# Kernel optimization log

Hardware: AMD Instinct MI355X
Metric: run time of the kernel (lower is better)

## Reference

```python
import jax, jax.numpy as jnp
import numpy as np

T, H, E = 1024, 2048, 32
I = 1024            # moe_intermediate_size
K = 8               # num_experts_per_token
G = 4               # num_expert_group
TOPK_GROUP = 2
N_SHARED = 2
IS = I * N_SHARED   # shared-expert intermediate
RSF = 2.5           # routed_scaling_factor


def setup_inputs() -> dict:
    key = jax.random.key(0)
    ks = jax.random.split(key, 9)
    s = 0.02
    return {
        "hidden_states": jax.random.normal(ks[0], (T, H), jnp.float32),
        "gate_w": jax.random.normal(ks[1], (H, E), jnp.float32) * s,
        "corr_bias": jax.random.normal(ks[2], (E,), jnp.float32) * s,
        "w_gate": jax.random.normal(ks[3], (E, H, I), jnp.float32) * s,
        "w_up": jax.random.normal(ks[4], (E, H, I), jnp.float32) * s,
        "w_down": jax.random.normal(ks[5], (E, I, H), jnp.float32) * s,
        "sw_gate": jax.random.normal(ks[6], (H, IS), jnp.float32) * s,
        "sw_up": jax.random.normal(ks[7], (H, IS), jnp.float32) * s,
        "sw_down": jax.random.normal(ks[8], (IS, H), jnp.float32) * s,
    }


def _route(x, gate_w, corr_bias):
    # biased grouped top-k (DeepSeek-V3 style sigmoid routing)
    logits = x @ gate_w                      # [T,E]
    scores = jax.nn.sigmoid(logits)
    sfc = scores + corr_bias[None, :]        # scores for choice
    grp = sfc.reshape(-1, G, E // G)
    # group score = sum of top-2 biased scores within the group
    grp_score = jax.lax.top_k(grp, 2)[0].sum(-1)          # [T,G]
    _, gidx = jax.lax.top_k(grp_score, TOPK_GROUP)        # [T,topk_group]
    rows = jnp.arange(sfc.shape[0])[:, None]
    gmask = jnp.zeros((sfc.shape[0], G), sfc.dtype).at[rows, gidx].set(1.0)
    emask = jnp.repeat(gmask, E // G, axis=1)             # [T,E]
    masked = jnp.where(emask > 0, sfc, -jnp.inf)
    _, idx = jax.lax.top_k(masked, K)                     # [T,K]
    w = jnp.take_along_axis(scores, idx, axis=1)          # unbiased scores
    w = w / w.sum(-1, keepdims=True)                      # renormalize
    w = w * RSF                                           # routed scaling
    combine = jnp.zeros((sfc.shape[0], E), x.dtype).at[rows, idx].add(w)
    return combine                                        # dense [T,E] combine weights


def reference(hidden_states, gate_w, corr_bias, w_gate, w_up, w_down,
              sw_gate, sw_up, sw_down):
    x = hidden_states
    # shared experts (SiLU-gated MLP)
    shared = (jax.nn.silu(x @ sw_gate) * (x @ sw_up)) @ sw_down   # [T,H]
    # routing
    combine = _route(x, gate_w, corr_bias)                        # [T,E]
    # routed experts (dense grouped-GEMM reference)
    g = jnp.einsum('th,ehi->tei', x, w_gate)
    u = jnp.einsum('th,ehi->tei', x, w_up)
    a = jax.nn.silu(g) * u                                        # [T,E,I]
    y = jnp.einsum('tei,eih->teh', a, w_down)                     # [T,E,H]
    routed = jnp.einsum('teh,te->th', y, combine)
    return routed + shared
```

## Files before the change

### kernel.cpp

```cpp
#include <hip/hip_runtime.h>

#define T_TOK 1024
#define H_DIM 2048
#define E_NUM 32
#define I_DIM 1024
#define IS_DIM 2048

typedef float  f32x4 __attribute__((ext_vector_type(4)));
typedef short  s16x8 __attribute__((ext_vector_type(8)));
typedef unsigned short u16x4 __attribute__((ext_vector_type(4)));
typedef unsigned short u16x8 __attribute__((ext_vector_type(8)));

__device__ __forceinline__ unsigned short f2bf(float f) {
    unsigned u = __builtin_bit_cast(unsigned, f);
    u = (u + 0x7fffu + ((u >> 16) & 1u)) >> 16;
    return (unsigned short)u;
}

__device__ __forceinline__ int swz(int r, int c) {
    return (r << 5) + (c ^ (((r >> 2) & 3) << 3));
}

__global__ __launch_bounds__(256) void cvt_k(
    const float* __restrict__ x, unsigned short* __restrict__ xb)
{
    const int i = (blockIdx.x * 256 + threadIdx.x) * 8;
    f32x4 a = *(const f32x4*)(x + i);
    f32x4 b = *(const f32x4*)(x + i + 4);
    u16x8 h = { f2bf(a[0]), f2bf(a[1]), f2bf(a[2]), f2bf(a[3]),
                f2bf(b[0]), f2bf(b[1]), f2bf(b[2]), f2bf(b[3]) };
    *(u16x8*)(xb + i) = h;
}

__global__ __launch_bounds__(256) void route_k(
    const float* __restrict__ x, const float* __restrict__ gw,
    const float* __restrict__ bias, int* __restrict__ tidx,
    float* __restrict__ tw)
{
    const int w = threadIdx.x >> 6;
    const int lane = threadIdx.x & 63;
    const int t = blockIdx.x * 4 + w;
    __shared__ float xs[4][H_DIM];
    __shared__ float sfc[4][E_NUM];
    __shared__ float sc[4][E_NUM];

    for (int i = threadIdx.x; i < 4 * (H_DIM / 4); i += 256) {
        int tt = i >> 9;
        int c = i & 511;
        *(f32x4*)&xs[tt][c * 4] =
            *(const f32x4*)(x + (size_t)(blockIdx.x * 4 + tt) * H_DIM + c * 4);
    }
    __syncthreads();

    const int eq = (lane & 7) * 4;
    const int hs = lane >> 3;
    f32x4 acc = {0.f, 0.f, 0.f, 0.f};
    #pragma unroll 4
    for (int h = hs; h < H_DIM; h += 8) {
        float xv = xs[w][h];
        f32x4 gv = *(const f32x4*)(gw + (size_t)h * E_NUM + eq);
        acc += gv * xv;
    }
    #pragma unroll
    for (int m = 8; m < 64; m <<= 1) {
        acc[0] += __shfl_xor(acc[0], m);
        acc[1] += __shfl_xor(acc[1], m);
        acc[2] += __shfl_xor(acc[2], m);
        acc[3] += __shfl_xor(acc[3], m);
    }
    if (lane < 8) {
        #pragma unroll
        for (int j = 0; j < 4; ++j) {
            float s = 1.f / (1.f + expf(-acc[j]));
            sc[w][eq + j] = s;
            sfc[w][eq + j] = s + bias[eq + j];
        }
    }
    __syncthreads();

    if (lane == 0) {
        float gs[4];
        for (int gg = 0; gg < 4; ++gg) {
            float m1 = -1e30f, m2 = -1e30f;
            for (int j = 0; j < 8; ++j) {
                float v = sfc[w][gg * 8 + j];
                if (v > m1) { m2 = m1; m1 = v; }
                else if (v > m2) { m2 = v; }
            }
            gs[gg] = m1 + m2;
        }
        int g1 = 0;
        for (int gg = 1; gg < 4; ++gg) if (gs[gg] > gs[g1]) g1 = gg;
        int g2 = (g1 == 0) ? 1 : 0;
        for (int gg = 0; gg < 4; ++gg)
            if (gg != g1 && gs[gg] > gs[g2]) g2 = gg;

        unsigned allow = (0xFFu << (g1 * 8)) | (0xFFu << (g2 * 8));
        unsigned taken = 0u;
        int   isel[8];
        float wsel[8];
        float wsum = 0.f;
        for (int k = 0; k < 8; ++k) {
            int best = 0; float bv = -1e30f;
            for (int e2 = 0; e2 < 32; ++e2) {
                if (((allow >> e2) & 1u) && !((taken >> e2) & 1u)) {
                    float v = sfc[w][e2];
                    if (v > bv) { bv = v; best = e2; }
                }
            }
            taken |= 1u << best;
            isel[k] = best;
            wsel[k] = sc[w][best];
            wsum += sc[w][best];
        }
        const float f = 2.5f / wsum;
        for (int k = 0; k < 8; ++k) {
            tidx[t * 8 + k] = isel[k];
            tw[t * 8 + k] = wsel[k] * f;
        }
    }
}

__global__ __launch_bounds__(64) void build_k(
    const int* __restrict__ tidx, const float* __restrict__ tw,
    int* __restrict__ ltok, float* __restrict__ lw, int* __restrict__ counts)
{
    const int e = blockIdx.x;
    const int lane = threadIdx.x;
    int cnt = 0;
    for (int t0 = 0; t0 < T_TOK; t0 += 64) {
        const int t = t0 + lane;
        int sel = 0; float w = 0.f;
        #pragma unroll
        for (int k = 0; k < 8; ++k) {
            if (tidx[t * 8 + k] == e) { sel = 1; w = tw[t * 8 + k]; }
        }
        unsigned long long m = __ballot(sel);
        int pos = __popcll(m & ((1ull << lane) - 1ull));
        if (sel) {
            ltok[e * T_TOK + cnt + pos] = t;
            lw[e * T_TOK + cnt + pos] = w;
        }
        cnt += __popcll(m);
    }
    if (lane == 0) counts[e] = cnt;
}

__global__ void prefix_k(const int* __restrict__ counts, int* __restrict__ offsets)
{
    if (threadIdx.x == 0) {
        int off = 0;
        for (int e = 0; e < E_NUM; ++e) { offsets[e] = off; off += counts[e]; }
    }
}

template<int DUAL, int EXPERT, int GATHER, int ATOMIC, int BM>
__global__ __launch_bounds__(256, 4) void gemm_k(
    const unsigned short* __restrict__ A, const float* __restrict__ B1g,
    const float* __restrict__ B2g, void* __restrict__ outv,
    const int* __restrict__ counts, const int* __restrict__ offsets,
    const int* __restrict__ ltok, const float* __restrict__ lw,
    int M, int N, int K)
{
    constexpr int WR  = BM / 2;
    constexpr int FM  = WR / 16;
    constexpr int TPR = 256 / BM;
    constexpr int KSP = 32 / TPR;
    constexpr int NB  = KSP / 8;

    const int e = blockIdx.z;
    const int Mloc = EXPERT ? counts[e] : M;
    const int col0 = blockIdx.y * 64;
    const int rb = EXPERT ? offsets[e] : 0;

    const float* B1 = B1g;
    const float* B2 = B2g;
    if (EXPERT) {
        size_t eo = (size_t)e * K * N;
        B1 += eo;
        if (DUAL) B2 += eo;
    }

    __shared__ unsigned short lA[2][BM * 32];
    __shared__ unsigned short lB[2][DUAL + 1][64 * 32];

    const int tid = threadIdx.x;
    const int lane = tid & 63;
    const int wv = tid >> 6;
    const int wm = wv >> 1;
    const int wn = wv & 1;

    const int arow = tid / TPR;
    const int akb  = (tid % TPR) * KSP;

    const bool doB = tid < (DUAL ? 256 : 128);
    const int bmat = DUAL ? (tid >> 7) : 0;
    const int t7 = tid & 127;
    const int nq = t7 & 15;
    const int kq = t7 >> 4;
    const float* bp = (bmat ? B2 : B1) + (size_t)(4 * kq) * N + col0 + nq * 4;

    f32x4 acc1[FM][2], acc2[FM][2];
    u16x8 pbaX[NB], pbaY[NB];
    f32x4 pbX[4], pbY[4];
    const unsigned short* apb = nullptr;

    auto loadT = [&](int k0, u16x8 (&pba)[NB], f32x4 (&pb)[4]) {
        #pragma unroll
        for (int i = 0; i < NB; ++i)
            pba[i] = *(const u16x8*)(apb + k0 + i * 8);
        if (doB) {
            #pragma unroll
            for (int j = 0; j < 4; ++j)
                pb[j] = *(const f32x4*)(bp + (size_t)(k0 + j) * N);
        }
    };

    auto storeT = [&](int p, u16x8 (&pba)[NB], f32x4 (&pb)[4]) {
        #pragma unroll
        for (int i = 0; i < NB; ++i)
            *(u16x8*)&lA[p][swz(arow, akb + i * 8)] = pba[i];
        if (doB) {
            #pragma unroll
            for (int j2 = 0; j2 < 4; ++j2) {
                u16x4 h = { f2bf(pb[0][j2]), f2bf(pb[1][j2]),
                            f2bf(pb[2][j2]), f2bf(pb[3][j2]) };
                *(u16x4*)&lB[p][bmat][swz(nq * 4 + j2, kq * 4)] = h;
            }
        }
    };

    auto compute = [&](int p) {
        const int koff = (lane >> 4) * 8;
        s16x8 af[FM], b1f[2], b2f[2];
        #pragma unroll
        for (int fm = 0; fm < FM; ++fm)
            af[fm] = *(const s16x8*)&lA[p][swz(wm * WR + fm * 16 + (lane & 15), koff)];
        #pragma unroll
        for (int fn = 0; fn < 2; ++fn) {
            b1f[fn] = *(const s16x8*)&lB[p][0][swz(wn * 32 + fn * 16 + (lane & 15), koff)];
            if (DUAL)
                b2f[fn] = *(const s16x8*)&lB[p][1][swz(wn * 32 + fn * 16 + (lane & 15), koff)];
        }
        #pragma unroll
        for (int fm = 0; fm < FM; ++fm)
            #pragma unroll
            for (int fn = 0; fn < 2; ++fn) {
                acc1[fm][fn] = __builtin_amdgcn_mfma_f32_16x16x32_bf16(
                    af[fm], b1f[fn], acc1[fm][fn], 0, 0, 0);
                if (DUAL)
                    acc2[fm][fn] = __builtin_amdgcn_mfma_f32_16x16x32_bf16(
                        af[fm], b2f[fn], acc2[fm][fn], 0, 0, 0);
            }
    };

    const int nk = K >> 5;

    for (int row0 = blockIdx.x * BM; row0 < Mloc; row0 += gridDim.x * BM) {
        {
            int rr = row0 + arow;
            if (rr >= Mloc) rr = Mloc - 1;
            int grow = GATHER ? ltok[e * T_TOK + rr] : (rb + rr);
            apb = A + (size_t)grow * K + akb;
        }
        #pragma unroll
        for (int a = 0; a < FM; ++a)
            #pragma unroll
            for (int b = 0; b < 2; ++b) {
                acc1[a][b] = f32x4{0.f, 0.f, 0.f, 0.f};
                acc2[a][b] = f32x4{0.f, 0.f, 0.f, 0.f};
            }

        loadT(0, pbaX, pbX);
        loadT(32, pbaY, pbY);
        __syncthreads();
        storeT(0, pbaX, pbX);
        __syncthreads();

        for (int kt = 0; kt < nk; kt += 2) {
            if (kt + 2 < nk) loadT((kt + 2) << 5, pbaX, pbX);
            compute(0);
            storeT(1, pbaY, pbY);
            __syncthreads();
            if (kt + 3 < nk) loadT((kt + 3) << 5, pbaY, pbY);
            compute(1);
            if (kt + 2 < nk) {
                storeT(0, pbaX, pbX);
                __syncthreads();
            }
        }

        const int fr = (lane >> 4) << 2;
        const int fc = lane & 15;
        if (DUAL) {
            unsigned short* outp = (unsigned short*)outv;
            #pragma unroll
            for (int fm = 0; fm < FM; ++fm)
                #pragma unroll
                for (int fn = 0; fn < 2; ++fn)
                    #pragma unroll
                    for (int j = 0; j < 4; ++j) {
                        int r = wm * WR + fm * 16 + fr + j;
                        if (row0 + r < Mloc) {
                            int cc = col0 + wn * 32 + fn * 16 + fc;
                            float gv = acc1[fm][fn][j];
                            float uv = acc2[fm][fn][j];
                            float a = gv / (1.f + expf(-gv)) * uv;
                            outp[(size_t)(rb + row0 + r) * N + cc] = f2bf(a);
                        }
                    }
        } else if (ATOMIC) {
            float* outp = (float*)outv;
            #pragma unroll
            for (int fm = 0; fm < FM; ++fm)
                #pragma unroll
                for (int fn = 0; fn < 2; ++fn)
                    #pragma unroll
                    for (int j = 0; j < 4; ++j) {
                        int r = wm * WR + fm * 16 + fr + j;
                        if (row0 + r < Mloc) {
                            int tok = ltok[e * T_TOK + row0 + r];
                            float wr = lw[e * T_TOK + row0 + r];
                            int cc = col0 + wn * 32 + fn * 16 + fc;
                            atomicAdd(outp + (size_t)tok * N + cc, acc1[fm][fn][j] * wr);
                        }
                    }
        } else {
            float* outp = (float*)outv;
            #pragma unroll
            for (int fm = 0; fm < FM; ++fm)
                #pragma unroll
                for (int fn = 0; fn < 2; ++fn)
                    #pragma unroll
                    for (int j = 0; j < 4; ++j) {
                        int r = wm * WR + fm * 16 + fr + j;
                        if (row0 + r < Mloc) {
                            int cc = col0 + wn * 32 + fn * 16 + fc;
                            outp[(size_t)(row0 + r) * N + cc] = acc1[fm][fn][j];
                        }
                    }
        }
    }
}

extern "C" void kernel_launch(void* const* d_in, const int* in_sizes, int n_in,
                              void* d_out, int out_size, void* d_ws, size_t ws_size,
                              hipStream_t stream) {
    const float* x       = (const float*)d_in[0];
    const float* gate_w  = (const float*)d_in[1];
    const float* bias    = (const float*)d_in[2];
    const float* w_gate  = (const float*)d_in[3];
    const float* w_up    = (const float*)d_in[4];
    const float* w_down  = (const float*)d_in[5];
    const float* sw_gate = (const float*)d_in[6];
    const float* sw_up   = (const float*)d_in[7];
    const float* sw_down = (const float*)d_in[8];
    float* out = (float*)d_out;

    char* ws = (char*)d_ws;
    int*   topk_idx = (int*)ws;
    float* topk_w   = (float*)(ws + 32768);
    int*   counts   = (int*)(ws + 65536);
    int*   offsets  = (int*)(ws + 65536 + 128);
    int*   ltok     = (int*)(ws + 65536 + 256);
    float* lw       = (float*)(ws + 65536 + 256 + 131072);
    unsigned short* act_s = (unsigned short*)(ws + 65536 + 256 + 262144);
    unsigned short* act_r = act_s + (size_t)T_TOK * IS_DIM;
    unsigned short* xbf   = act_r + (size_t)T_TOK * 8 * I_DIM;

    cvt_k<<<T_TOK * H_DIM / 2048, 256, 0, stream>>>(x, xbf);
    route_k<<<T_TOK / 4, 256, 0, stream>>>(x, gate_w, bias, topk_idx, topk_w);
    build_k<<<E_NUM, 64, 0, stream>>>(topk_idx, topk_w, ltok, lw, counts);
    prefix_k<<<1, 64, 0, stream>>>(counts, offsets);

    gemm_k<1,0,0,0,64><<<dim3(16, 32, 1), 256, 0, stream>>>(
        xbf, sw_gate, sw_up, act_s, nullptr, nullptr, nullptr, nullptr,
        T_TOK, IS_DIM, H_DIM);
    gemm_k<1,1,1,0,128><<<dim3(2, 16, 32), 256, 0, stream>>>(
        xbf, w_gate, w_up, act_r, counts, offsets, ltok, lw,
        T_TOK, I_DIM, H_DIM);
    gemm_k<0,0,0,0,64><<<dim3(16, 32, 1), 256, 0, stream>>>(
        act_s, sw_down, nullptr, out, nullptr, nullptr, nullptr, nullptr,
        T_TOK, H_DIM, IS_DIM);
    gemm_k<0,1,0,1,128><<<dim3(2, 32, 32), 256, 0, stream>>>(
        act_r, w_down, nullptr, out, counts, offsets, ltok, lw,
        T_TOK, H_DIM, I_DIM);
}
```

Measured before the change: 855.7 us.

## Replace atomic scatter with bf16 expert outputs and a separate combine kernel

```diff
diff --git a/kernel.cpp b/kernel.cpp
--- a/kernel.cpp
+++ b/kernel.cpp
@@ -16,9 +16,8 @@
     u = (u + 0x7fffu + ((u >> 16) & 1u)) >> 16;
     return (unsigned short)u;
 }
-
-__device__ __forceinline__ int swz(int r, int c) {
-    return (r << 5) + (c ^ (((r >> 2) & 3) << 3));
+__device__ __forceinline__ float bf2f(unsigned short h) {
+    return __builtin_bit_cast(float, (unsigned)h << 16);
 }
 
 __global__ __launch_bounds__(256) void cvt_k(
@@ -122,24 +121,24 @@
 }
 
 __global__ __launch_bounds__(64) void build_k(
-    const int* __restrict__ tidx, const float* __restrict__ tw,
-    int* __restrict__ ltok, float* __restrict__ lw, int* __restrict__ counts)
+    const int* __restrict__ tidx, int* __restrict__ ltok,
+    int* __restrict__ ppos, int* __restrict__ counts)
 {
     const int e = blockIdx.x;
     const int lane = threadIdx.x;
     int cnt = 0;
     for (int t0 = 0; t0 < T_TOK; t0 += 64) {
         const int t = t0 + lane;
-        int sel = 0; float w = 0.f;
+        int sel = 0, kk = 0;
         #pragma unroll
         for (int k = 0; k < 8; ++k) {
-            if (tidx[t * 8 + k] == e) { sel = 1; w = tw[t * 8 + k]; }
+            if (tidx[t * 8 + k] == e) { sel = 1; kk = k; }
         }
         unsigned long long m = __ballot(sel);
         int pos = __popcll(m & ((1ull << lane) - 1ull));
         if (sel) {
             ltok[e * T_TOK + cnt + pos] = t;
-            lw[e * T_TOK + cnt + pos] = w;
+            ppos[t * 8 + kk] = cnt + pos;
         }
         cnt += __popcll(m);
     }
@@ -154,22 +153,52 @@
     }
 }
 
-template<int DUAL, int EXPERT, int GATHER, int ATOMIC, int BM>
-__global__ __launch_bounds__(256, 4) void gemm_k(
-    const unsigned short* __restrict__ A, const float* __restrict__ B1g,
-    const float* __restrict__ B2g, void* __restrict__ outv,
+__global__ __launch_bounds__(256) void combine_k(
+    const int* __restrict__ tidx, const float* __restrict__ tw,
+    const int* __restrict__ offsets, const int* __restrict__ ppos,
+    const unsigned short* __restrict__ shd, const unsigned short* __restrict__ yd,
+    float* __restrict__ out)
+{
+    const int t = blockIdx.x;
+    const int h = threadIdx.x * 8;
+    u16x8 sv = *(const u16x8*)(shd + (size_t)t * H_DIM + h);
+    float a[8];
+    #pragma unroll
+    for (int j = 0; j < 8; ++j) a[j] = bf2f(sv[j]);
+    #pragma unroll
+    for (int k = 0; k < 8; ++k) {
+        int e = tidx[t * 8 + k];
+        float w = tw[t * 8 + k];
+        size_t row = (size_t)(offsets[e] + ppos[t * 8 + k]);
+        u16x8 v = *(const u16x8*)(yd + row * H_DIM + h);
+        #pragma unroll
+        for (int j = 0; j < 8; ++j) a[j] += w * bf2f(v[j]);
+    }
+    f32x4 lo = { a[0], a[1], a[2], a[3] };
+    f32x4 hi = { a[4], a[5], a[6], a[7] };
+    *(f32x4*)(out + (size_t)t * H_DIM + h)     = lo;
+    *(f32x4*)(out + (size_t)t * H_DIM + h + 4) = hi;
+}
+
+template<int DUAL, int EXPERT, int GATHER, int BM>
+__global__ __launch_bounds__(512) void gemm_k(
+    const unsigned short* __restrict__ A,
+    const float* __restrict__ B1g, const float* __restrict__ B2g,
+    unsigned short* __restrict__ outp,
     const int* __restrict__ counts, const int* __restrict__ offsets,
-    const int* __restrict__ ltok, const float* __restrict__ lw,
+    const int* __restrict__ ltok,
     int M, int N, int K)
 {
-    constexpr int WR  = BM / 2;
-    constexpr int FM  = WR / 16;
-    constexpr int TPR = 256 / BM;
+    constexpr int FM  = BM / 64;
+    constexpr int WR  = BM / 4;
+    constexpr int TPR = 512 / BM;
     constexpr int KSP = 32 / TPR;
     constexpr int NB  = KSP / 8;
 
     const int e = blockIdx.z;
     const int Mloc = EXPERT ? counts[e] : M;
+    const int row0 = blockIdx.x * BM;
+    if (row0 >= Mloc) return;
     const int col0 = blockIdx.y * 64;
     const int rb = EXPERT ? offsets[e] : 0;
 
@@ -181,8 +210,8 @@
         if (DUAL) B2 += eo;
     }
 
-    __shared__ unsigned short lA[2][BM * 32];
-    __shared__ unsigned short lB[2][DUAL + 1][64 * 32];
+    __shared__ unsigned short lA[2][BM][40];
+    __shared__ unsigned short lB[2][DUAL + 1][64][40];
 
     const int tid = threadIdx.x;
     const int lane = tid & 63;
@@ -192,6 +221,13 @@
 
     const int arow = tid / TPR;
     const int akb  = (tid % TPR) * KSP;
+    const unsigned short* apb;
+    {
+        int rr = row0 + arow;
+        if (rr >= Mloc) rr = Mloc - 1;
+        int grow = GATHER ? ltok[e * T_TOK + rr] : (rb + rr);
+        apb = A + (size_t)grow * K + akb;
+    }
 
     const bool doB = tid < (DUAL ? 256 : 128);
     const int bmat = DUAL ? (tid >> 7) : 0;
@@ -201,9 +237,16 @@
     const float* bp = (bmat ? B2 : B1) + (size_t)(4 * kq) * N + col0 + nq * 4;
 
     f32x4 acc1[FM][2], acc2[FM][2];
+    #pragma unroll
+    for (int a = 0; a < FM; ++a)
+        #pragma unroll
+        for (int b = 0; b < 2; ++b) {
+            acc1[a][b] = f32x4{0.f, 0.f, 0.f, 0.f};
+            acc2[a][b] = f32x4{0.f, 0.f, 0.f, 0.f};
+        }
+
     u16x8 pbaX[NB], pbaY[NB];
     f32x4 pbX[4], pbY[4];
-    const unsigned short* apb = nullptr;
 
     auto loadT = [&](int k0, u16x8 (&pba)[NB], f32x4 (&pb)[4]) {
         #pragma unroll
@@ -211,21 +254,24 @@
             pba[i] = *(const u16x8*)(apb + k0 + i * 8);
         if (doB) {
             #pragma unroll
-            for (int j = 0; j < 4; ++j)
-                pb[j] = *(const f32x4*)(bp + (size_t)(k0 + j) * N);
+            for (int j = 0; j < 4; ++j) {
+                const f32x4* src = (const f32x4*)(bp + (size_t)(k0 + j) * N);
+                if (EXPERT) pb[j] = __builtin_nontemporal_load(src);
+                else        pb[j] = *src;
+            }
         }
     };
 
     auto storeT = [&](int p, u16x8 (&pba)[NB], f32x4 (&pb)[4]) {
         #pragma unroll
         for (int i = 0; i < NB; ++i)
-            *(u16x8*)&lA[p][swz(arow, akb + i * 8)] = pba[i];
+            *(u16x8*)&lA[p][arow][akb + i * 8] = pba[i];
         if (doB) {
             #pragma unroll
             for (int j2 = 0; j2 < 4; ++j2) {
                 u16x4 h = { f2bf(pb[0][j2]), f2bf(pb[1][j2]),
                             f2bf(pb[2][j2]), f2bf(pb[3][j2]) };
-                *(u16x4*)&lB[p][bmat][swz(nq * 4 + j2, kq * 4)] = h;
+                *(u16x4*)&lB[p][bmat][nq * 4 + j2][kq * 4] = h;
             }
         }
     };
@@ -235,12 +281,12 @@
         s16x8 af[FM], b1f[2], b2f[2];
         #pragma unroll
         for (int fm = 0; fm < FM; ++fm)
-            af[fm] = *(const s16x8*)&lA[p][swz(wm * WR + fm * 16 + (lane & 15), koff)];
+            af[fm] = *(const s16x8*)&lA[p][wm * WR + fm * 16 + (lane & 15)][koff];
         #pragma unroll
         for (int fn = 0; fn < 2; ++fn) {
-            b1f[fn] = *(const s16x8*)&lB[p][0][swz(wn * 32 + fn * 16 + (lane & 15), koff)];
+            b1f[fn] = *(const s16x8*)&lB[p][0][wn * 32 + fn * 16 + (lane & 15)][koff];
             if (DUAL)
-                b2f[fn] = *(const s16x8*)&lB[p][1][swz(wn * 32 + fn * 16 + (lane & 15), koff)];
+                b2f[fn] = *(const s16x8*)&lB[p][1][wn * 32 + fn * 16 + (lane & 15)][koff];
         }
         #pragma unroll
         for (int fm = 0; fm < FM; ++fm)
@@ -255,92 +301,46 @@
     };
 
     const int nk = K >> 5;
-
-    for (int row0 = blockIdx.x * BM; row0 < Mloc; row0 += gridDim.x * BM) {
-        {
-            int rr = row0 + arow;
-            if (rr >= Mloc) rr = Mloc - 1;
-            int grow = GATHER ? ltok[e * T_TOK + rr] : (rb + rr);
-            apb = A + (size_t)grow * K + akb;
-        }
-        #pragma unroll
-        for (int a = 0; a < FM; ++a)
+    loadT(0, pbaX, pbX);
+    loadT(32, pbaY, pbY);
+    storeT(0, pbaX, pbX);
+    __syncthreads();
+
+    for (int kt = 0; kt < nk; kt += 2) {
+        if (kt + 2 < nk) loadT((kt + 2) << 5, pbaX, pbX);
+        compute(0);
+        storeT(1, pbaY, pbY);
+        __syncthreads();
+        if (kt + 3 < nk) loadT((kt + 3) << 5, pbaY, pbY);
+        compute(1);
+        if (kt + 2 < nk) {
+            storeT(0, pbaX, pbX);
+            __syncthreads();
+        }
+    }
+
+    const int fr = (lane >> 4) << 2;
+    const int fc = lane & 15;
+    #pragma unroll
+    for (int fm = 0; fm < FM; ++fm)
+        #pragma unroll
+        for (int fn = 0; fn < 2; ++fn)
             #pragma unroll
-            for (int b = 0; b < 2; ++b) {
-                acc1[a][b] = f32x4{0.f, 0.f, 0.f, 0.f};
-                acc2[a][b] = f32x4{0.f, 0.f, 0.f, 0.f};
-            }
-
-        loadT(0, pbaX, pbX);
-        loadT(32, pbaY, pbY);
-        __syncthreads();
-        storeT(0, pbaX, pbX);
-        __syncthreads();
-
-        for (int kt = 0; kt < nk; kt += 2) {
-            if (kt + 2 < nk) loadT((kt + 2) << 5, pbaX, pbX);
-            compute(0);
-            storeT(1, pbaY, pbY);
-            __syncthreads();
-            if (kt + 3 < nk) loadT((kt + 3) << 5, pbaY, pbY);
-            compute(1);
-            if (kt + 2 < nk) {
-                storeT(0, pbaX, pbX);
-                __syncthreads();
-            }
-        }
-
-        const int fr = (lane >> 4) << 2;
-        const int fc = lane & 15;
-        if (DUAL) {
-            unsigned short* outp = (unsigned short*)outv;
-            #pragma unroll
-            for (int fm = 0; fm < FM; ++fm)
-                #pragma unroll
-                for (int fn = 0; fn < 2; ++fn)
-                    #pragma unroll
-                    for (int j = 0; j < 4; ++j) {
-                        int r = wm * WR + fm * 16 + fr + j;
-                        if (row0 + r < Mloc) {
-                            int cc = col0 + wn * 32 + fn * 16 + fc;
-                            float gv = acc1[fm][fn][j];
-                            float uv = acc2[fm][fn][j];
-                            float a = gv / (1.f + expf(-gv)) * uv;
-                            outp[(size_t)(rb + row0 + r) * N + cc] = f2bf(a);
-                        }
+            for (int j = 0; j < 4; ++j) {
+                int r = wm * WR + fm * 16 + fr + j;
+                if (row0 + r < Mloc) {
+                    int cc = col0 + wn * 32 + fn * 16 + fc;
+                    float v;
+                    if (DUAL) {
+                        float gv = acc1[fm][fn][j];
+                        float uv = acc2[fm][fn][j];
+                        v = gv / (1.f + expf(-gv)) * uv;
+                    } else {
+                        v = acc1[fm][fn][j];
                     }
-        } else if (ATOMIC) {
-            float* outp = (float*)outv;
-            #pragma unroll
-            for (int fm = 0; fm < FM; ++fm)
-                #pragma unroll
-                for (int fn = 0; fn < 2; ++fn)
-                    #pragma unroll
-                    for (int j = 0; j < 4; ++j) {
-                        int r = wm * WR + fm * 16 + fr + j;
-                        if (row0 + r < Mloc) {
-                            int tok = ltok[e * T_TOK + row0 + r];
-                            float wr = lw[e * T_TOK + row0 + r];
-                            int cc = col0 + wn * 32 + fn * 16 + fc;
-                            atomicAdd(outp + (size_t)tok * N + cc, acc1[fm][fn][j] * wr);
-                        }
-                    }
-        } else {
-            float* outp = (float*)outv;
-            #pragma unroll
-            for (int fm = 0; fm < FM; ++fm)
-                #pragma unroll
-                for (int fn = 0; fn < 2; ++fn)
-                    #pragma unroll
-                    for (int j = 0; j < 4; ++j) {
-                        int r = wm * WR + fm * 16 + fr + j;
-                        if (row0 + r < Mloc) {
-                            int cc = col0 + wn * 32 + fn * 16 + fc;
-                            outp[(size_t)(row0 + r) * N + cc] = acc1[fm][fn][j];
-                        }
-                    }
-        }
-    }
+                    outp[(size_t)(rb + row0 + r) * N + cc] = f2bf(v);
+                }
+            }
 }
 
 extern "C" void kernel_launch(void* const* d_in, const int* in_sizes, int n_in,
@@ -361,28 +361,33 @@
     int*   topk_idx = (int*)ws;
     float* topk_w   = (float*)(ws + 32768);
     int*   counts   = (int*)(ws + 65536);
-    int*   offsets  = (int*)(ws + 65536 + 128);
-    int*   ltok     = (int*)(ws + 65536 + 256);
-    float* lw       = (float*)(ws + 65536 + 256 + 131072);
-    unsigned short* act_s = (unsigned short*)(ws + 65536 + 256 + 262144);
-    unsigned short* act_r = act_s + (size_t)T_TOK * IS_DIM;
-    unsigned short* xbf   = act_r + (size_t)T_TOK * 8 * I_DIM;
+    int*   offsets  = (int*)(ws + 65664);
+    int*   ppos     = (int*)(ws + 65792);
+    int*   ltok     = (int*)(ws + 98560);
+    unsigned short* xbf   = (unsigned short*)(ws + 262144);
+    unsigned short* act_s = xbf + (size_t)T_TOK * H_DIM;
+    unsigned short* shd   = act_s + (size_t)T_TOK * IS_DIM;
+    unsigned short* act_r = shd + (size_t)T_TOK * H_DIM;
+    unsigned short* yd    = act_r + (size_t)T_TOK * 8 * I_DIM;
 
     cvt_k<<<T_TOK * H_DIM / 2048, 256, 0, stream>>>(x, xbf);
     route_k<<<T_TOK / 4, 256, 0, stream>>>(x, gate_w, bias, topk_idx, topk_w);
-    build_k<<<E_NUM, 64, 0, stream>>>(topk_idx, topk_w, ltok, lw, counts);
+    build_k<<<E_NUM, 64, 0, stream>>>(topk_idx, ltok, ppos, counts);
     prefix_k<<<1, 64, 0, stream>>>(counts, offsets);
 
-    gemm_k<1,0,0,0,64><<<dim3(16, 32, 1), 256, 0, stream>>>(
-        xbf, sw_gate, sw_up, act_s, nullptr, nullptr, nullptr, nullptr,
+    gemm_k<1,0,0,128><<<dim3(8, 32, 1), 512, 0, stream>>>(
+        xbf, sw_gate, sw_up, act_s, nullptr, nullptr, nullptr,
         T_TOK, IS_DIM, H_DIM);
-    gemm_k<1,1,1,0,128><<<dim3(2, 16, 32), 256, 0, stream>>>(
-        xbf, w_gate, w_up, act_r, counts, offsets, ltok, lw,
+    gemm_k<1,1,1,256><<<dim3(4, 16, 32), 512, 0, stream>>>(
+        xbf, w_gate, w_up, act_r, counts, offsets, ltok,
         T_TOK, I_DIM, H_DIM);
-    gemm_k<0,0,0,0,64><<<dim3(16, 32, 1), 256, 0, stream>>>(
-        act_s, sw_down, nullptr, out, nullptr, nullptr, nullptr, nullptr,
+    gemm_k<0,0,0,128><<<dim3(8, 32, 1), 512, 0, stream>>>(
+        act_s, sw_down, nullptr, shd, nullptr, nullptr, nullptr,
         T_TOK, H_DIM, IS_DIM);
-    gemm_k<0,1,0,1,128><<<dim3(2, 32, 32), 256, 0, stream>>>(
-        act_r, w_down, nullptr, out, counts, offsets, ltok, lw,
+    gemm_k<0,1,0,256><<<dim3(4, 32, 32), 512, 0, stream>>>(
+        act_r, w_down, nullptr, yd, counts, offsets, ltok,
         T_TOK, H_DIM, I_DIM);
-}
+
+    combine_k<<<T_TOK, 256, 0, stream>>>(
+        topk_idx, topk_w, offsets, ppos, shd, yd, out);
+}
```

Result: slower. 1.018 ms (+18.9%).
